# Performance work log

Hardware: AMD Instinct MI355X
Metric: run time of the kernel (lower is better)

The kernel has to match this reference:

```python
import jax, jax.numpy as jnp
import numpy as np
from jax import lax

B, C, H, W = 8, 256, 32, 32
NH = 8            # num_heads
HID = 4 * C       # mlp hidden
EPS = 1e-5        # BatchNorm eps


def setup_inputs() -> dict:
    key = jax.random.key(0)
    ks = jax.random.split(key, 16)
    s = 1.0 / np.sqrt(C)
    return {
        "x1": jax.random.normal(ks[0], (B, C, H, W), jnp.float32),
        "x2": jax.random.normal(ks[1], (B, C, H, W), jnp.float32),
        # norm1 (shared for x1 and x2), eval-mode BatchNorm params
        "bn1_g": jax.random.uniform(ks[2], (C,), jnp.float32, 0.5, 1.5),
        "bn1_b": jax.random.normal(ks[3], (C,), jnp.float32) * 0.1,
        "bn1_m": jax.random.normal(ks[4], (C,), jnp.float32) * 0.1,
        "bn1_v": jax.random.uniform(ks[5], (C,), jnp.float32, 0.5, 1.5),
        # attention 1x1 convs (bias=False) + proj (with bias)
        "q_w": jax.random.normal(ks[6], (C, C), jnp.float32) * s,
        "k_w": jax.random.normal(ks[7], (C, C), jnp.float32) * s,
        "v_w": jax.random.normal(ks[8], (C, C), jnp.float32) * s,
        "temp": jnp.ones((NH,), jnp.float32),
        "proj_w": jax.random.normal(ks[9], (C, C), jnp.float32) * s,
        "proj_b": jnp.zeros((C,), jnp.float32),
        # norm2
        "bn2_g": jax.random.uniform(ks[10], (C,), jnp.float32, 0.5, 1.5),
        "bn2_b": jax.random.normal(ks[11], (C,), jnp.float32) * 0.1,
        "bn2_m": jax.random.normal(ks[12], (C,), jnp.float32) * 0.1,
        "bn2_v": jax.random.uniform(ks[13], (C,), jnp.float32, 0.5, 1.5),
        # MLP: fc1 (1x1), depthwise 3x3 (no bias), fc2 (1x1)
        "fc1_w": jax.random.normal(ks[14], (HID, C), jnp.float32) * s,
        "fc1_b": jnp.zeros((HID,), jnp.float32),
        "dw_w": jax.random.normal(ks[15], (HID, 1, 3, 3), jnp.float32) * (1.0 / 3.0),
        "fc2_w": jax.random.normal(jax.random.fold_in(key, 99), (C, HID), jnp.float32) * (1.0 / np.sqrt(HID)),
        "fc2_b": jnp.zeros((C,), jnp.float32),
    }


def _bn(x, g, b, m, v):
    # eval-mode BatchNorm2d over channel dim
    inv = g * lax.rsqrt(v + EPS)
    return x * inv[None, :, None, None] + (b - m * inv)[None, :, None, None]


def _conv1x1(x, w, b=None):
    y = jnp.einsum('oc,bchw->bohw', w, x)
    if b is not None:
        y = y + b[None, :, None, None]
    return y


def _attn(x1n, x2n, q_w, k_w, v_w, temp, proj_w, proj_b):
    d = C // NH
    hw = H * W
    q = _conv1x1(x1n, q_w).reshape(B, NH, d, hw).transpose(0, 1, 3, 2)  # [B,h,HW,d]
    k = _conv1x1(x2n, k_w).reshape(B, NH, d, hw)                        # [B,h,d,HW]
    v = _conv1x1(x2n, v_w).reshape(B, NH, d, hw).transpose(0, 1, 3, 2)  # [B,h,HW,d]
    attn = jnp.einsum('bhnd,bhdm->bhnm', q, k) * temp[None, :, None, None]
    attn = jax.nn.softmax(attn, axis=-1)       # dropout = identity (eval)
    out = jnp.einsum('bhnm,bhmd->bhnd', attn, v)
    out = out.transpose(0, 1, 3, 2).reshape(B, C, H, W)
    return _conv1x1(out, proj_w, proj_b)


def _mlp(x, fc1_w, fc1_b, dw_w, fc2_w, fc2_b):
    h = _conv1x1(x, fc1_w, fc1_b)
    h = lax.conv_general_dilated(h, dw_w, (1, 1), 'SAME',
                                 dimension_numbers=('NCHW', 'OIHW', 'NCHW'),
                                 feature_group_count=HID)
    h = jax.nn.gelu(h, approximate=False)
    return _conv1x1(h, fc2_w, fc2_b)


def reference(x1, x2, bn1_g, bn1_b, bn1_m, bn1_v, q_w, k_w, v_w, temp, proj_w,
              proj_b, bn2_g, bn2_b, bn2_m, bn2_v, fc1_w, fc1_b, dw_w, fc2_w, fc2_b):
    x1 = x1 + _attn(_bn(x1, bn1_g, bn1_b, bn1_m, bn1_v),
                    _bn(x2, bn1_g, bn1_b, bn1_m, bn1_v),
                    q_w, k_w, v_w, temp, proj_w, proj_b)
    x1 = x1 + _mlp(_bn(x1, bn2_g, bn2_b, bn2_m, bn2_v),
                   fc1_w, fc1_b, dw_w, fc2_w, fc2_b)
    return x1
```

## Files before the change

### kernel.cpp

```cpp
#include <hip/hip_runtime.h>
#include <math.h>

#define HW    1024
#define CCH   256
#define NHEAD 8
#define HIDC  1024
#define BATCH 8
#define L2E   1.44269504f

typedef unsigned short u16;
typedef __attribute__((ext_vector_type(8))) short  bf16x8;
typedef __attribute__((ext_vector_type(4))) float  f32x4;
typedef __attribute__((ext_vector_type(8))) unsigned short us8;
typedef __attribute__((ext_vector_type(4))) unsigned short us4;

__device__ __forceinline__ u16 f2b(float f) {
    union { float f; unsigned u; } c; c.f = f;
    unsigned r = c.u + 0x7FFFu + ((c.u >> 16) & 1u);
    return (u16)(r >> 16);
}
__device__ __forceinline__ float b2f(u16 u) {
    union { unsigned u; float f; } c; c.u = ((unsigned)u) << 16;
    return c.f;
}
__device__ __forceinline__ unsigned cvt_pk_bf16(float a, float b) {
    unsigned r;
    asm volatile("v_cvt_pk_bf16_f32 %0, %1, %2" : "=v"(r) : "v"(a), "v"(b));
    return r;
}

__global__ void bn_coef_kernel(const float* __restrict__ g1, const float* __restrict__ b1,
                               const float* __restrict__ m1, const float* __restrict__ v1,
                               const float* __restrict__ g2, const float* __restrict__ b2,
                               const float* __restrict__ m2, const float* __restrict__ v2,
                               const float* __restrict__ temp, float* __restrict__ coef) {
    int c = threadIdx.x;
    if (c < CCH) {
        float i1 = g1[c] * rsqrtf(v1[c] + 1e-5f);
        coef[c]        = i1;
        coef[256 + c]  = b1[c] - m1[c] * i1;
        float i2 = g2[c] * rsqrtf(v2[c] + 1e-5f);
        coef[512 + c]  = i2;
        coef[768 + c]  = b2[c] - m2[c] * i2;
        coef[1024 + c] = temp[c >> 5] * L2E;
    }
}

__global__ __launch_bounds__(256)
void cvt_all(const float* __restrict__ qw, const float* __restrict__ kw,
             const float* __restrict__ vw, const float* __restrict__ pw,
             const float* __restrict__ f1, const float* __restrict__ f2,
             u16* __restrict__ dst) {
    int bid = blockIdx.x;
    const float* src; size_t off; int lb;
    if      (bid < 64)  { src = qw; off = 0;      lb = bid; }
    else if (bid < 128) { src = kw; off = 65536;  lb = bid - 64; }
    else if (bid < 192) { src = vw; off = 131072; lb = bid - 128; }
    else if (bid < 256) { src = pw; off = 196608; lb = bid - 192; }
    else if (bid < 512) { src = f1; off = 262144; lb = bid - 256; }
    else                { src = f2; off = 524288; lb = bid - 512; }
    int i = lb * 1024 + threadIdx.x * 4;
    float4 v = *(const float4*)(src + i);
    us4 o = { f2b(v.x), f2b(v.y), f2b(v.z), f2b(v.w) };
    *(us4*)(dst + off + i) = o;
}

__global__ __launch_bounds__(256)
void dwt_kernel(const float* __restrict__ dw, u16* __restrict__ dwt) {
    int idx = blockIdx.x * 256 + threadIdx.x;
    if (idx < 9 * HIDC) {
        int t = idx >> 10, c = idx & 1023;
        dwt[t * HIDC + c] = f2b(dw[c * 9 + t]);
    }
}

__global__ __launch_bounds__(256)
void xbn_t_kernel(const float* __restrict__ x1, const float* __restrict__ x2,
                  const float* __restrict__ a, const float* __restrict__ be,
                  u16* __restrict__ o1, u16* __restrict__ o2) {
    __shared__ alignas(16) u16 lt[64 * 72];
    int z = blockIdx.z;
    const float* x = (z & 1) ? x2 : x1;
    u16* o = (z & 1) ? o2 : o1;
    int b = z >> 1;
    int n0 = blockIdx.x * 64, c0 = blockIdx.y * 64;
    const float* xb = x + ((size_t)b * CCH + c0) * HW + n0;
    int tid = threadIdx.x;
    int row = tid >> 4, col4 = (tid & 15) * 4;
#pragma unroll
    for (int it = 0; it < 4; ++it) {
        int rr = it * 16 + row;
        float sc = a[c0 + rr], sh = be[c0 + rr];
        float4 v = *(const float4*)(xb + (size_t)rr * HW + col4);
        lt[(col4 + 0) * 72 + rr] = f2b(v.x * sc + sh);
        lt[(col4 + 1) * 72 + rr] = f2b(v.y * sc + sh);
        lt[(col4 + 2) * 72 + rr] = f2b(v.z * sc + sh);
        lt[(col4 + 3) * 72 + rr] = f2b(v.w * sc + sh);
    }
    __syncthreads();
    u16* ob = o + ((size_t)b * HW + n0) * CCH + c0;
#pragma unroll
    for (int rep = 0; rep < 2; ++rep) {
        int idx = tid * 2 + rep;
        int nl = idx >> 3, slot = idx & 7;
        us8 v = *(const us8*)(&lt[nl * 72 + slot * 8]);
        *(us8*)(ob + (size_t)nl * CCH + slot * 8) = v;
    }
}

__device__ __forceinline__ void stage_pair(const u16* Xb, const u16* Wb, int K, int koff,
                                           u16* lx, u16* lw, int wv, int lane) {
    int rl = lane >> 3, slot = lane & 7;
#pragma unroll
    for (int r = 0; r < 2; ++r) {
        int region = wv * 2 + r;
        int row = region * 8 + rl;
        int sw = ((slot ^ (row & 7)) << 3) + koff;
        __builtin_amdgcn_global_load_lds(
            (const __attribute__((address_space(1))) void*)(Xb + (size_t)row * K + sw),
            (__attribute__((address_space(3))) void*)(lx + (region << 9)), 16, 0, 0);
        __builtin_amdgcn_global_load_lds(
            (const __attribute__((address_space(1))) void*)(Wb + (size_t)row * K + sw),
            (__attribute__((address_space(3))) void*)(lw + (region << 9)), 16, 0, 0);
    }
}

__device__ __forceinline__ void compute_tile(const u16* lx, const u16* lw,
                                             int cc, int g, int wr, int wc,
                                             f32x4 acc[2][2]) {
#pragma unroll
    for (int ks = 0; ks < 2; ++ks) {
        bf16x8 ax[2], bw[2];
#pragma unroll
        for (int mi = 0; mi < 2; ++mi) {
            int row = wr * 32 + mi * 16 + cc;
            int ck = (ks * 4 + g) ^ (row & 7);
            ax[mi] = *(const bf16x8*)(lx + row * 64 + ck * 8);
        }
#pragma unroll
        for (int ni = 0; ni < 2; ++ni) {
            int row = wc * 32 + ni * 16 + cc;
            int ck = (ks * 4 + g) ^ (row & 7);
            bw[ni] = *(const bf16x8*)(lw + row * 64 + ck * 8);
        }
#pragma unroll
        for (int mi = 0; mi < 2; ++mi)
#pragma unroll
            for (int ni = 0; ni < 2; ++ni)
                acc[mi][ni] = __builtin_amdgcn_mfma_f32_16x16x32_bf16(
                    ax[mi], bw[ni], acc[mi][ni], 0, 0, 0);
    }
}

__global__ __launch_bounds__(256, 4)
void gemm_nhwc(const u16* __restrict__ W, const u16* __restrict__ X,
               const float* __restrict__ bias, const float* __restrict__ resid,
               float* __restrict__ outf, u16* __restrict__ outb,
               const float* __restrict__ bn_a, const float* __restrict__ bn_be,
               int K, int M) {
    __shared__ alignas(16) u16 lx[2][4096];
    __shared__ alignas(16) u16 lw[2][4096];
    const int tid = threadIdx.x, l = tid & 63, wv = tid >> 6;
    const int cc = l & 15, g = l >> 4;
    const int wr = wv >> 1, wc = wv & 1;
    const int n0 = blockIdx.x * 64, m0 = blockIdx.y * 64, b = blockIdx.z;
    const u16* Xb = X + ((size_t)b * HW + n0) * K;
    const u16* Wb = W + (size_t)m0 * K;
    const size_t bo = (size_t)b * M * HW;
    if (resid) resid += bo;
    if (outf)  outf  += bo;
    if (outb)  outb  += (size_t)b * HW * M;

    f32x4 acc[2][2];
    acc[0][0] = (f32x4)0.f; acc[0][1] = (f32x4)0.f;
    acc[1][0] = (f32x4)0.f; acc[1][1] = (f32x4)0.f;

    const int NT = K >> 6;
    stage_pair(Xb, Wb, K, 0, lx[0], lw[0], wv, l);
    __syncthreads();
    int cur = 0;
    for (int t = 0; t < NT; ++t) {
        if (t + 1 < NT)
            stage_pair(Xb, Wb, K, (t + 1) * 64, lx[cur ^ 1], lw[cur ^ 1], wv, l);
        compute_tile(lx[cur], lw[cur], cc, g, wr, wc, acc);
        __syncthreads();
        cur ^= 1;
    }

#pragma unroll
    for (int mi = 0; mi < 2; ++mi)
#pragma unroll
        for (int ni = 0; ni < 2; ++ni) {
            int m  = m0 + wc * 32 + ni * 16 + cc;
            int nb = n0 + wr * 32 + mi * 16 + g * 4;
            f32x4 v = acc[mi][ni];
            if (bias) { float bv = bias[m]; v[0] += bv; v[1] += bv; v[2] += bv; v[3] += bv; }
            if (resid) {
                float4 rv = *(const float4*)(resid + (size_t)m * HW + nb);
                v[0] += rv.x; v[1] += rv.y; v[2] += rv.z; v[3] += rv.w;
            }
            if (outf) *(f32x4*)(outf + (size_t)m * HW + nb) = v;
            if (outb) {
                float sa = bn_a ? bn_a[m] : 1.0f;
                float sb = bn_a ? bn_be[m] : 0.0f;
#pragma unroll
                for (int r = 0; r < 4; ++r)
                    outb[(size_t)(nb + r) * M + m] = f2b(v[r] * sa + sb);
            }
        }
}

__global__ __launch_bounds__(256, 4)
void qkv_gemm(const u16* __restrict__ wq, const u16* __restrict__ wk,
              const u16* __restrict__ wv, const u16* __restrict__ x1n,
              const u16* __restrict__ x2n, const float* __restrict__ tscale,
              u16* __restrict__ qt, u16* __restrict__ kt, u16* __restrict__ vbuf) {
    __shared__ alignas(16) u16 lx[2][4096];
    __shared__ alignas(16) u16 lw[2][4096];
    const int tid = threadIdx.x, l = tid & 63, wvv = tid >> 6;
    const int cc = l & 15, g = l >> 4;
    const int wr = wvv >> 1, wc = wvv & 1;
    const int sel = blockIdx.y >> 2;
    const int n0 = blockIdx.x * 64, m0 = (blockIdx.y & 3) * 64, b = blockIdx.z;
    const u16* W = (sel == 0) ? wq : (sel == 1) ? wk : wv;
    const u16* Xb = ((sel == 0) ? x1n : x2n) + ((size_t)b * HW + n0) * CCH;
    const u16* Wb = W + (size_t)m0 * CCH;

    f32x4 acc[2][2];
    acc[0][0] = (f32x4)0.f; acc[0][1] = (f32x4)0.f;
    acc[1][0] = (f32x4)0.f; acc[1][1] = (f32x4)0.f;

    stage_pair(Xb, Wb, CCH, 0, lx[0], lw[0], wvv, l);
    __syncthreads();
    int cur = 0;
    for (int t = 0; t < 4; ++t) {
        if (t + 1 < 4)
            stage_pair(Xb, Wb, CCH, (t + 1) * 64, lx[cur ^ 1], lw[cur ^ 1], wvv, l);
        compute_tile(lx[cur], lw[cur], cc, g, wr, wc, acc);
        __syncthreads();
        cur ^= 1;
    }

    if (sel < 2) {
        u16* ob = ((sel == 0) ? qt : kt) + (size_t)b * HW * CCH;
#pragma unroll
        for (int mi = 0; mi < 2; ++mi)
#pragma unroll
            for (int ni = 0; ni < 2; ++ni) {
                int m  = m0 + wc * 32 + ni * 16 + cc;
                int nb = n0 + wr * 32 + mi * 16 + g * 4;
                float sc = (sel == 0) ? tscale[m] : 1.0f;
#pragma unroll
                for (int r = 0; r < 4; ++r)
                    ob[(size_t)(nb + r) * CCH + m] = f2b(acc[mi][ni][r] * sc);
            }
    } else {
        u16* ob = vbuf + (size_t)b * CCH * HW;
#pragma unroll
        for (int mi = 0; mi < 2; ++mi)
#pragma unroll
            for (int ni = 0; ni < 2; ++ni) {
                int m  = m0 + wc * 32 + ni * 16 + cc;
                int nb = n0 + wr * 32 + mi * 16 + g * 4;
                us4 ov = { f2b(acc[mi][ni][0]), f2b(acc[mi][ni][1]),
                           f2b(acc[mi][ni][2]), f2b(acc[mi][ni][3]) };
                *(us4*)(ob + (size_t)m * HW + nb) = ov;
            }
    }
}

#define ATT_LOAD(K0, K1, K2, K3, V0, V1, V2, V3, T) do {                      \
    const int j0_ = (T) * 64;                                                 \
    K0 = *(const bf16x8*)(kb + (size_t)(j0_ +  0 + c) * CCH + g * 8);         \
    K1 = *(const bf16x8*)(kb + (size_t)(j0_ + 16 + c) * CCH + g * 8);         \
    K2 = *(const bf16x8*)(kb + (size_t)(j0_ + 32 + c) * CCH + g * 8);         \
    K3 = *(const bf16x8*)(kb + (size_t)(j0_ + 48 + c) * CCH + g * 8);         \
    V0 = *(const bf16x8*)(vb + (size_t)( 0 + c) * HW + j0_ +  0 + g * 8);     \
    V1 = *(const bf16x8*)(vb + (size_t)(16 + c) * HW + j0_ +  0 + g * 8);     \
    V2 = *(const bf16x8*)(vb + (size_t)( 0 + c) * HW + j0_ + 32 + g * 8);     \
    V3 = *(const bf16x8*)(vb + (size_t)(16 + c) * HW + j0_ + 32 + g * 8);     \
} while (0)

#define ATT_COMP(K0, K1, K2, K3, V0, V1, V2, V3) do {                         \
    f32x4 s0[4], s1[4];                                                       \
    __builtin_amdgcn_s_setprio(1);                                            \
    s0[0] = __builtin_amdgcn_mfma_f32_16x16x32_bf16(K0, qf0, (f32x4)0.f, 0, 0, 0); \
    s1[0] = __builtin_amdgcn_mfma_f32_16x16x32_bf16(K0, qf1, (f32x4)0.f, 0, 0, 0); \
    s0[1] = __builtin_amdgcn_mfma_f32_16x16x32_bf16(K1, qf0, (f32x4)0.f, 0, 0, 0); \
    s1[1] = __builtin_amdgcn_mfma_f32_16x16x32_bf16(K1, qf1, (f32x4)0.f, 0, 0, 0); \
    s0[2] = __builtin_amdgcn_mfma_f32_16x16x32_bf16(K2, qf0, (f32x4)0.f, 0, 0, 0); \
    s1[2] = __builtin_amdgcn_mfma_f32_16x16x32_bf16(K2, qf1, (f32x4)0.f, 0, 0, 0); \
    s0[3] = __builtin_amdgcn_mfma_f32_16x16x32_bf16(K3, qf0, (f32x4)0.f, 0, 0, 0); \
    s1[3] = __builtin_amdgcn_mfma_f32_16x16x32_bf16(K3, qf1, (f32x4)0.f, 0, 0, 0); \
    __builtin_amdgcn_s_setprio(0);                                            \
    float pm0 = -3.0e38f, pm1 = -3.0e38f;                                     \
    _Pragma("unroll")                                                         \
    for (int nj = 0; nj < 4; ++nj)                                            \
        _Pragma("unroll")                                                     \
        for (int r = 0; r < 4; ++r) {                                         \
            pm0 = fmaxf(pm0, s0[nj][r]);                                      \
            pm1 = fmaxf(pm1, s1[nj][r]);                                      \
        }                                                                     \
    pm0 = fmaxf(pm0, __shfl_xor(pm0, 16));                                    \
    pm0 = fmaxf(pm0, __shfl_xor(pm0, 32));                                    \
    pm1 = fmaxf(pm1, __shfl_xor(pm1, 16));                                    \
    pm1 = fmaxf(pm1, __shfl_xor(pm1, 32));                                    \
    if (!__all((pm0 <= rm0 + 8.0f) && (pm1 <= rm1 + 8.0f))) {                 \
        float mn0 = fmaxf(rm0, pm0), scl0 = exp2f(rm0 - mn0);                 \
        float mn1 = fmaxf(rm1, pm1), scl1 = exp2f(rm1 - mn1);                 \
        rm0 = mn0; rm1 = mn1;                                                 \
        rl0 *= scl0; rl1 *= scl1;                                             \
        _Pragma("unroll")                                                     \
        for (int r = 0; r < 4; ++r) {                                         \
            int src = (l & 48) | (g * 4 + r);                                 \
            float so0 = __shfl(scl0, src);                                    \
            float so1 = __shfl(scl1, src);                                    \
            o00[r] *= so0; o01[r] *= so0;                                     \
            o10[r] *= so1; o11[r] *= so1;                                     \
        }                                                                     \
    }                                                                         \
    float ps0 = 0.f, ps1 = 0.f;                                               \
    _Pragma("unroll")                                                         \
    for (int nj = 0; nj < 4; ++nj) {                                          \
        int ck = (2 * nj + (g >> 1)) ^ swz;                                   \
        float a0 = exp2f(s0[nj][0] - rm0), a1 = exp2f(s0[nj][1] - rm0);       \
        float a2 = exp2f(s0[nj][2] - rm0), a3 = exp2f(s0[nj][3] - rm0);       \
        ps0 += (a0 + a1) + (a2 + a3);                                         \
        uint2 pk0;                                                            \
        pk0.x = cvt_pk_bf16(a0, a1);                                          \
        pk0.y = cvt_pk_bf16(a2, a3);                                          \
        *(uint2*)(&P[c * 64 + ck * 8 + (g & 1) * 4]) = pk0;                   \
        float d0 = exp2f(s1[nj][0] - rm1), d1 = exp2f(s1[nj][1] - rm1);       \
        float d2 = exp2f(s1[nj][2] - rm1), d3 = exp2f(s1[nj][3] - rm1);       \
        ps1 += (d0 + d1) + (d2 + d3);                                         \
        uint2 pk1;                                                            \
        pk1.x = cvt_pk_bf16(d0, d1);                                          \
        pk1.y = cvt_pk_bf16(d2, d3);                                          \
        *(uint2*)(&P[(16 + c) * 64 + ck * 8 + (g & 1) * 4]) = pk1;            \
    }                                                                         \
    rl0 += ps0; rl1 += ps1;                                                   \
    asm volatile("s_waitcnt lgkmcnt(0)" ::: "memory");                        \
    __builtin_amdgcn_sched_barrier(0);                                        \
    __builtin_amdgcn_s_setprio(1);                                            \
    _Pragma("unroll")                                                         \
    for (int kj = 0; kj < 2; ++kj) {                                          \
        bf16x8 pf0 = *(const bf16x8*)(&P[c * 64 + ((kj * 4 + g) ^ swz) * 8]); \
        bf16x8 pf1 = *(const bf16x8*)(&P[(16 + c) * 64 + ((kj * 4 + g) ^ swz) * 8]); \
        o00 = __builtin_amdgcn_mfma_f32_16x16x32_bf16(pf0, (kj ? V2 : V0), o00, 0, 0, 0); \
        o01 = __builtin_amdgcn_mfma_f32_16x16x32_bf16(pf0, (kj ? V3 : V1), o01, 0, 0, 0); \
        o10 = __builtin_amdgcn_mfma_f32_16x16x32_bf16(pf1, (kj ? V2 : V0), o10, 0, 0, 0); \
        o11 = __builtin_amdgcn_mfma_f32_16x16x32_bf16(pf1, (kj ? V3 : V1), o11, 0, 0, 0); \
    }                                                                         \
    __builtin_amdgcn_s_setprio(0);                                            \
} while (0)

__global__ __launch_bounds__(256)
void attn_mfma(const u16* __restrict__ qt, const u16* __restrict__ kt,
               const u16* __restrict__ vv, u16* __restrict__ out) {
    __shared__ alignas(16) u16 lds[8192];
    const int tid = threadIdx.x, l = tid & 63, w = tid >> 6;
    const int c = l & 15, g = l >> 4;
    const int swz = (c & 7) ^ ((c & 8) >> 1);
    const int bh = blockIdx.x & 63, qx = blockIdx.x >> 6;
    const int b = bh >> 3, h = bh & 7;
    const int n0 = qx * 128;
    u16* P = lds + w * 2048;

    const u16* qb = qt + ((size_t)b * HW + n0 + w * 32) * CCH + h * 32;
    const u16* kb = kt + (size_t)b * HW * CCH + h * 32;
    const u16* vb = vv + ((size_t)b * CCH + h * 32) * HW;

    bf16x8 qf0 = *(const bf16x8*)(qb + (size_t)c * CCH + g * 8);
    bf16x8 qf1 = *(const bf16x8*)(qb + (size_t)(16 + c) * CCH + g * 8);

    float rm0 = -3.0e38f, rm1 = -3.0e38f, rl0 = 0.f, rl1 = 0.f;
    f32x4 o00 = (f32x4)0.f, o01 = (f32x4)0.f;
    f32x4 o10 = (f32x4)0.f, o11 = (f32x4)0.f;

    bf16x8 kA0, kA1, kA2, kA3, vA0, vA1, vA2, vA3;
    bf16x8 kB0, kB1, kB2, kB3, vB0, vB1, vB2, vB3;

    ATT_LOAD(kA0, kA1, kA2, kA3, vA0, vA1, vA2, vA3, 0);
#pragma unroll 1
    for (int t = 0; t < 16; t += 2) {
        ATT_LOAD(kB0, kB1, kB2, kB3, vB0, vB1, vB2, vB3, t + 1);
        ATT_COMP(kA0, kA1, kA2, kA3, vA0, vA1, vA2, vA3);
        if (t + 2 < 16)
            ATT_LOAD(kA0, kA1, kA2, kA3, vA0, vA1, vA2, vA3, t + 2);
        ATT_COMP(kB0, kB1, kB2, kB3, vB0, vB1, vB2, vB3);
    }

    rl0 += __shfl_xor(rl0, 16); rl0 += __shfl_xor(rl0, 32);
    rl1 += __shfl_xor(rl1, 16); rl1 += __shfl_xor(rl1, 32);
    float inv0 = 1.0f / rl0, inv1 = 1.0f / rl1;
    float invr0[4], invr1[4];
#pragma unroll
    for (int r = 0; r < 4; ++r) {
        int src = (l & 48) | (g * 4 + r);
        invr0[r] = __shfl(inv0, src);
        invr1[r] = __shfl(inv1, src);
    }
    asm volatile("s_waitcnt lgkmcnt(0)" ::: "memory");
    __builtin_amdgcn_sched_barrier(0);
#pragma unroll
    for (int r = 0; r < 4; ++r) {
        int row0 = g * 4 + r, row1 = 16 + g * 4 + r;
        P[row0 * 40 + c]      = f2b(o00[r] * invr0[r]);
        P[row0 * 40 + 16 + c] = f2b(o01[r] * invr0[r]);
        P[row1 * 40 + c]      = f2b(o10[r] * invr1[r]);
        P[row1 * 40 + 16 + c] = f2b(o11[r] * invr1[r]);
    }
    asm volatile("s_waitcnt lgkmcnt(0)" ::: "memory");
    __builtin_amdgcn_sched_barrier(0);
#pragma unroll
    for (int rep = 0; rep < 2; ++rep) {
        int u = l * 2 + rep;
        int i = u >> 2, part = u & 3;
        us8 ov = *(const us8*)(&P[i * 40 + part * 8]);
        *(us8*)(out + ((size_t)b * HW + n0 + w * 32 + i) * CCH + h * 32 + part * 8) = ov;
    }
}

__global__ __launch_bounds__(256)
void dwgelu_nhwc(const u16* __restrict__ in, const u16* __restrict__ wt,
                 u16* __restrict__ out) {
    int gid = blockIdx.x * 256 + threadIdx.x;
    int c0 = (gid & 127) * 8;
    int sp = (gid >> 7) & 1023;
    int b  = gid >> 17;
    int y = sp >> 5, x = sp & 31;
    const u16* ip = in + (size_t)b * HW * HIDC;
    float acc[8] = {0.f, 0.f, 0.f, 0.f, 0.f, 0.f, 0.f, 0.f};
#pragma unroll
    for (int dy = -1; dy <= 1; ++dy) {
        int yy = y + dy;
        if ((unsigned)yy >= 32u) continue;
#pragma unroll
        for (int dx = -1; dx <= 1; ++dx) {
            int xx = x + dx;
            if ((unsigned)xx >= 32u) continue;
            us8 iv = *(const us8*)(ip + (size_t)(yy * 32 + xx) * HIDC + c0);
            us8 wv = *(const us8*)(wt + ((dy + 1) * 3 + dx + 1) * HIDC + c0);
#pragma unroll
            for (int e = 0; e < 8; ++e)
                acc[e] = fmaf(b2f(wv[e]), b2f(iv[e]), acc[e]);
        }
    }
    us8 o;
#pragma unroll
    for (int e = 0; e < 8; ++e) {
        float ge = 0.5f * acc[e] * (1.0f + erff(acc[e] * 0.70710678118f));
        o[e] = f2b(ge);
    }
    *(us8*)(out + (size_t)gid * 8) = o;
}

extern "C" void kernel_launch(void* const* d_in, const int* in_sizes, int n_in,
                              void* d_out, int out_size, void* d_ws, size_t ws_size,
                              hipStream_t stream) {
    const float* x1     = (const float*)d_in[0];
    const float* x2     = (const float*)d_in[1];
    const float* bn1_g  = (const float*)d_in[2];
    const float* bn1_b  = (const float*)d_in[3];
    const float* bn1_m  = (const float*)d_in[4];
    const float* bn1_v  = (const float*)d_in[5];
    const float* q_w    = (const float*)d_in[6];
    const float* k_w    = (const float*)d_in[7];
    const float* v_w    = (const float*)d_in[8];
    const float* temp   = (const float*)d_in[9];
    const float* proj_w = (const float*)d_in[10];
    const float* proj_b = (const float*)d_in[11];
    const float* bn2_g  = (const float*)d_in[12];
    const float* bn2_b  = (const float*)d_in[13];
    const float* bn2_m  = (const float*)d_in[14];
    const float* bn2_v  = (const float*)d_in[15];
    const float* fc1_w  = (const float*)d_in[16];
    const float* fc1_b  = (const float*)d_in[17];
    const float* dw_w   = (const float*)d_in[18];
    const float* fc2_w  = (const float*)d_in[19];
    const float* fc2_b  = (const float*)d_in[20];

    const size_t SZ = (size_t)BATCH * CCH * HW;
    float* coef = (float*)d_ws;
    u16*   bp   = (u16*)(coef + 2048);
    u16* qwb   = bp;
    u16* kwb   = bp + 65536;
    u16* vwb   = bp + 131072;
    u16* pjwb  = bp + 196608;
    u16* fc1wb = bp + 262144;
    u16* fc2wb = bp + 524288;
    u16* dwt   = bp + 786432;
    u16* act   = bp + 802816;
    u16* x1n   = act;
    u16* x2n   = act + SZ;
    u16* qtb   = act + 2 * SZ;
    u16* ktb   = act + 3 * SZ;
    u16* vbuf  = act + 4 * SZ;
    u16* attnb = act + 5 * SZ;
    float* y1  = (float*)(act + 6 * SZ);
    u16* y1n   = act + 8 * SZ;
    u16* h1    = act + 9 * SZ;
    u16* h2    = act + 13 * SZ;

    bn_coef_kernel<<<1, 256, 0, stream>>>(bn1_g, bn1_b, bn1_m, bn1_v,
                                          bn2_g, bn2_b, bn2_m, bn2_v, temp, coef);
    cvt_all<<<768, 256, 0, stream>>>(q_w, k_w, v_w, proj_w, fc1_w, fc2_w, bp);
    dwt_kernel<<<36, 256, 0, stream>>>(dw_w, dwt);
    xbn_t_kernel<<<dim3(16, 4, 16), 256, 0, stream>>>(x1, x2, coef, coef + 256,
                                                      x1n, x2n);

    qkv_gemm<<<dim3(16, 12, BATCH), 256, 0, stream>>>(qwb, kwb, vwb, x1n, x2n,
                                                      coef + 1024, qtb, ktb, vbuf);

    attn_mfma<<<512, 256, 0, stream>>>(qtb, ktb, vbuf, attnb);

    gemm_nhwc<<<dim3(16, 4, BATCH), 256, 0, stream>>>(pjwb, attnb, proj_b, x1,
                                                      y1, y1n, coef + 512, coef + 768,
                                                      CCH, CCH);
    gemm_nhwc<<<dim3(16, 16, BATCH), 256, 0, stream>>>(fc1wb, y1n, fc1_b, nullptr,
                                                       nullptr, h1, nullptr, nullptr,
                                                       CCH, HIDC);
    dwgelu_nhwc<<<(BATCH * HW * HIDC / 8) / 256, 256, 0, stream>>>(h1, dwt, h2);

    gemm_nhwc<<<dim3(16, 4, BATCH), 256, 0, stream>>>(fc2wb, h2, fc2_b, y1,
                                                      (float*)d_out, nullptr,
                                                      nullptr, nullptr, HIDC, CCH);
}
```

Baseline: 125.7 us.

## Split attention KV loop in two and merge partials in a combine kernel

The attention kernel now splits the key/value sequence into two halves across separate blocks, doubling the grid from 512 to 1024 blocks. Each block writes unnormalized fp32 partial outputs plus the running max and sum, and a new combine kernel rescales and merges them into bf16. The aim is better occupancy of the GPU's compute units for a grid that was small. The cost is extra fp32 traffic for the partials, one more kernel launch, and a larger workspace.

```diff
diff --git a/kernel.cpp b/kernel.cpp
--- a/kernel.cpp
+++ b/kernel.cpp
@@ -355,13 +355,14 @@
 } while (0)
 
 __global__ __launch_bounds__(256)
-void attn_mfma(const u16* __restrict__ qt, const u16* __restrict__ kt,
-               const u16* __restrict__ vv, u16* __restrict__ out) {
+void attn_part(const u16* __restrict__ qt, const u16* __restrict__ kt,
+               const u16* __restrict__ vv, float* __restrict__ pO,
+               float2* __restrict__ pml) {
     __shared__ alignas(16) u16 lds[8192];
     const int tid = threadIdx.x, l = tid & 63, w = tid >> 6;
     const int c = l & 15, g = l >> 4;
     const int swz = (c & 7) ^ ((c & 8) >> 1);
-    const int bh = blockIdx.x & 63, qx = blockIdx.x >> 6;
+    const int bh = blockIdx.x & 63, qx = (blockIdx.x >> 6) & 7, sp = blockIdx.x >> 9;
     const int b = bh >> 3, h = bh & 7;
     const int n0 = qx * 128;
     u16* P = lds + w * 2048;
@@ -380,45 +381,61 @@
     bf16x8 kA0, kA1, kA2, kA3, vA0, vA1, vA2, vA3;
     bf16x8 kB0, kB1, kB2, kB3, vB0, vB1, vB2, vB3;
 
-    ATT_LOAD(kA0, kA1, kA2, kA3, vA0, vA1, vA2, vA3, 0);
+    const int t0 = sp * 8;
+    ATT_LOAD(kA0, kA1, kA2, kA3, vA0, vA1, vA2, vA3, t0);
 #pragma unroll 1
-    for (int t = 0; t < 16; t += 2) {
+    for (int t = t0; t < t0 + 8; t += 2) {
         ATT_LOAD(kB0, kB1, kB2, kB3, vB0, vB1, vB2, vB3, t + 1);
         ATT_COMP(kA0, kA1, kA2, kA3, vA0, vA1, vA2, vA3);
-        if (t + 2 < 16)
+        if (t + 2 < t0 + 8)
             ATT_LOAD(kA0, kA1, kA2, kA3, vA0, vA1, vA2, vA3, t + 2);
         ATT_COMP(kB0, kB1, kB2, kB3, vB0, vB1, vB2, vB3);
     }
 
     rl0 += __shfl_xor(rl0, 16); rl0 += __shfl_xor(rl0, 32);
     rl1 += __shfl_xor(rl1, 16); rl1 += __shfl_xor(rl1, 32);
-    float inv0 = 1.0f / rl0, inv1 = 1.0f / rl1;
-    float invr0[4], invr1[4];
-#pragma unroll
-    for (int r = 0; r < 4; ++r) {
-        int src = (l & 48) | (g * 4 + r);
-        invr0[r] = __shfl(inv0, src);
-        invr1[r] = __shfl(inv1, src);
-    }
-    asm volatile("s_waitcnt lgkmcnt(0)" ::: "memory");
-    __builtin_amdgcn_sched_barrier(0);
+
+    float* po = pO + (((size_t)sp * 64 + bh) * HW + n0 + w * 32) * 32;
 #pragma unroll
     for (int r = 0; r < 4; ++r) {
         int row0 = g * 4 + r, row1 = 16 + g * 4 + r;
-        P[row0 * 40 + c]      = f2b(o00[r] * invr0[r]);
-        P[row0 * 40 + 16 + c] = f2b(o01[r] * invr0[r]);
-        P[row1 * 40 + c]      = f2b(o10[r] * invr1[r]);
-        P[row1 * 40 + 16 + c] = f2b(o11[r] * invr1[r]);
-    }
-    asm volatile("s_waitcnt lgkmcnt(0)" ::: "memory");
-    __builtin_amdgcn_sched_barrier(0);
-#pragma unroll
-    for (int rep = 0; rep < 2; ++rep) {
-        int u = l * 2 + rep;
-        int i = u >> 2, part = u & 3;
-        us8 ov = *(const us8*)(&P[i * 40 + part * 8]);
-        *(us8*)(out + ((size_t)b * HW + n0 + w * 32 + i) * CCH + h * 32 + part * 8) = ov;
-    }
+        po[row0 * 32 + c]      = o00[r];
+        po[row0 * 32 + 16 + c] = o01[r];
+        po[row1 * 32 + c]      = o10[r];
+        po[row1 * 32 + 16 + c] = o11[r];
+    }
+    if (g == 0) {
+        float2* pp = pml + ((size_t)sp * 64 + bh) * HW + n0 + w * 32;
+        pp[c]      = make_float2(rm0, rl0);
+        pp[16 + c] = make_float2(rm1, rl1);
+    }
+}
+
+__global__ __launch_bounds__(256)
+void attn_comb(const float* __restrict__ pO, const float2* __restrict__ pml,
+               u16* __restrict__ out) {
+    int gid = blockIdx.x * 256 + threadIdx.x;
+    int dp  = (gid & 3) * 8;
+    int row = gid >> 2;
+    int bh = row >> 10, n = row & 1023;
+    int b = bh >> 3, h = bh & 7;
+    float2 ml0 = pml[row];
+    float2 ml1 = pml[(size_t)64 * HW + row];
+    float M  = fmaxf(ml0.x, ml1.x);
+    float w0 = exp2f(ml0.x - M), w1 = exp2f(ml1.x - M);
+    float inv = 1.0f / (ml0.y * w0 + ml1.y * w1);
+    float a0 = w0 * inv, a1 = w1 * inv;
+    const float* p0 = pO + (size_t)row * 32 + dp;
+    const float* p1 = p0 + (size_t)64 * HW * 32;
+    f32x4 x0 = *(const f32x4*)p0, x1 = *(const f32x4*)(p0 + 4);
+    f32x4 y0 = *(const f32x4*)p1, y1 = *(const f32x4*)(p1 + 4);
+    us8 o;
+#pragma unroll
+    for (int e = 0; e < 4; ++e) {
+        o[e]     = f2b(x0[e] * a0 + y0[e] * a1);
+        o[4 + e] = f2b(x1[e] * a0 + y1[e] * a1);
+    }
+    *(us8*)(out + ((size_t)b * HW + n) * CCH + h * 32 + dp) = o;
 }
 
 __global__ __launch_bounds__(256)
@@ -501,6 +518,8 @@
     u16* y1n   = act + 8 * SZ;
     u16* h1    = act + 9 * SZ;
     u16* h2    = act + 13 * SZ;
+    float*  pO  = (float*)(act + 17 * SZ);
+    float2* pml = (float2*)(pO + 2 * 64 * HW * 32);
 
     bn_coef_kernel<<<1, 256, 0, stream>>>(bn1_g, bn1_b, bn1_m, bn1_v,
                                           bn2_g, bn2_b, bn2_m, bn2_v, temp, coef);
@@ -512,7 +531,8 @@
     qkv_gemm<<<dim3(16, 12, BATCH), 256, 0, stream>>>(qwb, kwb, vwb, x1n, x2n,
                                                       coef + 1024, qtb, ktb, vbuf);
 
-    attn_mfma<<<512, 256, 0, stream>>>(qtb, ktb, vbuf, attnb);
+    attn_part<<<1024, 256, 0, stream>>>(qtb, ktb, vbuf, pO, pml);
+    attn_comb<<<1024, 256, 0, stream>>>(pO, pml, attnb);
 
     gemm_nhwc<<<dim3(16, 4, BATCH), 256, 0, stream>>>(pjwb, attnb, proj_b, x1,
                                                       y1, y1n, coef + 512, coef + 768,
```

Measured after the change: 133.4 us. 1.06x slower.
